# Kernel optimization log

Measured on AMD Instinct MI355X. Metric: run time of the kernel, lower is better.

Reference implementation:

```python
import jax, jax.numpy as jnp
import numpy as np

STD = 0.01

def setup_inputs() -> dict:
    key = jax.random.key(0)
    k1, k2, k3 = jax.random.split(key, 3)
    B, T, D = 16, 4096, 512
    x = jax.random.normal(k1, (B, T, D), dtype=jnp.float32)
    att_W = jax.random.normal(k2, (D, D), dtype=jnp.float32) * STD
    att_v = jax.random.normal(k3, (D,), dtype=jnp.float32) * STD
    return {"x": x, "att_W": att_W, "att_v": att_v}

def reference(x, att_W, att_v):
    # additive attention scores: tanh(x @ W) @ v -> [B, T]
    y = jnp.tanh(jnp.einsum('btd,de->bte', x, att_W))
    scores = jnp.einsum('btd,d->bt', y, att_v)
    weights = jax.nn.softmax(scores, axis=-1)          # softmax over sequence
    out = jnp.einsum('bt,btd->bd', weights, x)         # weighted sum pooling
    return out.astype(jnp.float32)
```

## Files before the change

kernel.cpp:

```cpp
#include <hip/hip_runtime.h>
#include <hip/hip_bf16.h>
#include <math.h>

#define BB 16
#define TT 4096
#define DD 512
#define MM (BB*TT)

typedef __bf16 bf16x8 __attribute__((ext_vector_type(8)));
typedef float  f32x4  __attribute__((ext_vector_type(4)));

__device__ inline unsigned short f2bf(float f) {
    unsigned u = __builtin_bit_cast(unsigned, f) + 0x8000u;
    return (unsigned short)(u >> 16);
}

__device__ inline unsigned pack_bf16x2(float lo, float hi) {
    unsigned u0 = __builtin_bit_cast(unsigned, lo) + 0x8000u;
    unsigned u1 = __builtin_bit_cast(unsigned, hi) + 0x8000u;
    return __builtin_amdgcn_perm(u1, u0, 0x07060302);
}

__device__ inline float tanh_fast(float y) {
    float e = __expf(2.0f * y);
    return 1.0f - 2.0f * __builtin_amdgcn_rcpf(e + 1.0f);
}

__global__ void wb_kernel(const float* __restrict__ W, unsigned short* __restrict__ Wb) {
    int u = blockIdx.x * 256 + threadIdx.x;
    int lane = u & 63;
    int fid  = u >> 6;
    int ni = fid & 1;
    int s  = (fid >> 1) & 15;
    int p  = (fid >> 5) & 7;
    int h  = fid >> 8;
    int n  = h * 256 + p * 32 + ni * 16 + (lane & 15);
    int k0 = s * 32 + (lane >> 4) * 8;
    unsigned short o[8];
    #pragma unroll
    for (int j = 0; j < 8; j++) o[j] = f2bf(W[(size_t)(k0 + j) * DD + n]);
    *(uint4*)(Wb + (size_t)u * 8) = *(uint4*)o;
}

__global__ __launch_bounds__(256, 2) void scorepool_kernel(
        const float* __restrict__ x, const unsigned short* __restrict__ Wb,
        const float* __restrict__ v,
        float* __restrict__ num_ws, float* __restrict__ mz_ws) {
    __shared__ unsigned short As[64 * DD];
    __shared__ float sbuf[4][64];
    __shared__ float ew[64];
    __shared__ float mzsh[2];
    __shared__ float psum[4][DD];

    const int tid  = threadIdx.x;
    const int m0   = blockIdx.x * 64;
    const int wid  = tid >> 6;
    const int lane = tid & 63;
    const int l15  = lane & 15;
    const int q    = lane >> 4;
    const int r3   = l15 & 7;
    const int wh   = wid;

    ((float*)sbuf)[tid] = 0.f;

    #pragma unroll 4
    for (int i = 0; i < 16; i++) {
        int u = i * 256 + tid;
        int r = u >> 6;
        int c = u & 63;
        const float* gp = x + (size_t)(m0 + r) * DD + c * 8;
        f32x4 f0 = __builtin_nontemporal_load((const f32x4*)(gp));
        f32x4 f1 = __builtin_nontemporal_load((const f32x4*)(gp + 4));
        uint4 o;
        o.x = pack_bf16x2(f0.x, f0.y);
        o.y = pack_bf16x2(f0.z, f0.w);
        o.z = pack_bf16x2(f1.x, f1.y);
        o.w = pack_bf16x2(f1.z, f1.w);
        *(uint4*)(&As[r * DD + (c ^ (r & 7)) * 8]) = o;
    }

    const unsigned short* bqp = Wb + (size_t)wh * 65536 + lane * 8;
    bf16x8 b[4][2];
    #pragma unroll
    for (int g = 0; g < 3; g++) {
        b[g][0] = *(const bf16x8*)(bqp);
        b[g][1] = *(const bf16x8*)(bqp + 512);
        bqp += 1024;
    }

    __syncthreads();

#define A_FRAG(mi, s) (*(const bf16x8*)(&As[((mi)*16 + l15) * DD + ((((s)*4 + q) ^ r3) * 8)]))

    bf16x8 a[2][4];
    #pragma unroll
    for (int mi = 0; mi < 4; mi++) a[0][mi] = A_FRAG(mi, 0);

    #pragma unroll 1
    for (int p = 0; p < 4; p++) {
        f32x4 acc[4][2];
        #pragma unroll
        for (int mi = 0; mi < 4; mi++) {
            acc[mi][0] = (f32x4){0.f, 0.f, 0.f, 0.f};
            acc[mi][1] = (f32x4){0.f, 0.f, 0.f, 0.f};
        }

        #pragma unroll
        for (int s = 0; s < 16; s++) {
            const int ns = (s + 1) & 15;
            #pragma unroll
            for (int mi = 0; mi < 4; mi++) a[(s + 1) & 1][mi] = A_FRAG(mi, ns);
            b[(s + 3) & 3][0] = *(const bf16x8*)(bqp);
            b[(s + 3) & 3][1] = *(const bf16x8*)(bqp + 512);
            bqp += 1024;
            #pragma unroll
            for (int mi = 0; mi < 4; mi++)
                #pragma unroll
                for (int ni = 0; ni < 2; ni++)
                    acc[mi][ni] = __builtin_amdgcn_mfma_f32_16x16x32_bf16(
                        a[s & 1][mi], b[s & 3][ni], acc[mi][ni], 0, 0, 0);
        }

        float vv0 = v[wh * 128 + p * 32 + l15];
        float vv1 = v[wh * 128 + p * 32 + 16 + l15];
        #pragma unroll
        for (int mi = 0; mi < 4; mi++)
            #pragma unroll
            for (int rr = 0; rr < 4; rr++) {
                float sum = tanh_fast(acc[mi][0][rr]) * vv0
                          + tanh_fast(acc[mi][1][rr]) * vv1;
                sum += __shfl_xor(sum, 1);
                sum += __shfl_xor(sum, 2);
                sum += __shfl_xor(sum, 4);
                sum += __shfl_xor(sum, 8);
                if (l15 == 0)
                    sbuf[wh][mi * 16 + q * 4 + rr] += sum;
            }
    }
#undef A_FRAG

    __syncthreads();

    if (tid < 64) {
        float s = sbuf[0][tid] + sbuf[1][tid] + sbuf[2][tid] + sbuf[3][tid];
        float m = s;
        #pragma unroll
        for (int off = 32; off; off >>= 1) m = fmaxf(m, __shfl_xor(m, off));
        float e = __expf(s - m);
        float z = e;
        #pragma unroll
        for (int off = 32; off; off >>= 1) z += __shfl_xor(z, off);
        ew[tid] = e;
        if (tid == 0) { mzsh[0] = m; mzsh[1] = z; }
    }
    __syncthreads();

    const int cx = tid & 63;
    const int rg = tid >> 6;
    float nacc[8];
    #pragma unroll
    for (int j = 0; j < 8; j++) nacc[j] = 0.f;
    #pragma unroll 4
    for (int i = 0; i < 16; i++) {
        int r = rg * 16 + i;
        uint4 u = *(const uint4*)(&As[r * DD + ((cx ^ (r & 7)) * 8)]);
        float e = ew[r];
        nacc[0] += e * __builtin_bit_cast(float, u.x << 16);
        nacc[1] += e * __builtin_bit_cast(float, u.x & 0xFFFF0000u);
        nacc[2] += e * __builtin_bit_cast(float, u.y << 16);
        nacc[3] += e * __builtin_bit_cast(float, u.y & 0xFFFF0000u);
        nacc[4] += e * __builtin_bit_cast(float, u.z << 16);
        nacc[5] += e * __builtin_bit_cast(float, u.z & 0xFFFF0000u);
        nacc[6] += e * __builtin_bit_cast(float, u.w << 16);
        nacc[7] += e * __builtin_bit_cast(float, u.w & 0xFFFF0000u);
    }
    *(float4*)(&psum[rg][cx * 8])     = *(float4*)(&nacc[0]);
    *(float4*)(&psum[rg][cx * 8 + 4]) = *(float4*)(&nacc[4]);
    __syncthreads();

    if (tid < 128) {
        int c = tid * 4;
        f32x4 f = *(const f32x4*)(&psum[0][c]);
        f += *(const f32x4*)(&psum[1][c]);
        f += *(const f32x4*)(&psum[2][c]);
        f += *(const f32x4*)(&psum[3][c]);
        __builtin_nontemporal_store(f, (f32x4*)(num_ws + (size_t)blockIdx.x * DD + c));
    }
    if (tid == 0) {
        mz_ws[2 * blockIdx.x]     = mzsh[0];
        mz_ws[2 * blockIdx.x + 1] = mzsh[1];
    }
}

__global__ void combine_kernel(const float* __restrict__ num_ws,
                               const float* __restrict__ mz_ws,
                               float* __restrict__ out) {
    __shared__ float fs[64];
    __shared__ float sinv_sh;
    const int b   = blockIdx.x;
    const int tid = threadIdx.x;

    if (tid < 64) {
        float m = mz_ws[(b * 64 + tid) * 2];
        float z = mz_ws[(b * 64 + tid) * 2 + 1];
        float M = m;
        #pragma unroll
        for (int off = 32; off; off >>= 1) M = fmaxf(M, __shfl_xor(M, off));
        float f  = __expf(m - M);
        float fz = f * z;
        #pragma unroll
        for (int off = 32; off; off >>= 1) fz += __shfl_xor(fz, off);
        fs[tid] = f;
        if (tid == 0) sinv_sh = 1.0f / fz;
    }
    __syncthreads();

    float a0 = 0.f, a1 = 0.f;
    #pragma unroll 4
    for (int c = 0; c < 64; c++) {
        float f = fs[c];
        const float* np = num_ws + (size_t)(b * 64 + c) * DD;
        a0 += f * np[tid];
        a1 += f * np[tid + 256];
    }
    const float sinv = sinv_sh;
    out[b * DD + tid]       = a0 * sinv;
    out[b * DD + tid + 256] = a1 * sinv;
}

extern "C" void kernel_launch(void* const* d_in, const int* in_sizes, int n_in,
                              void* d_out, int out_size, void* d_ws, size_t ws_size,
                              hipStream_t stream) {
    (void)in_sizes; (void)n_in; (void)out_size; (void)ws_size;
    const float* x = (const float*)d_in[0];
    const float* W = (const float*)d_in[1];
    const float* v = (const float*)d_in[2];
    float* out = (float*)d_out;

    unsigned short* Wb = (unsigned short*)d_ws;
    float* num_ws      = (float*)((char*)d_ws + 512 * 1024 + 16 * 1024);
    float* mz_ws       = (float*)((char*)d_ws + 512 * 1024 + 16 * 1024 + 2 * 1024 * 1024);

    wb_kernel<<<128, 256, 0, stream>>>(W, Wb);

    scorepool_kernel<<<MM / 64, 256, 0, stream>>>(x, Wb, v, num_ws, mz_ws);

    combine_kernel<<<BB, 256, 0, stream>>>(num_ws, mz_ws, out);
}
```

Before: 301.6 us.

## Switch score GEMM to 32x32x16 bf16 MFMA with deeper operand prefetch

Replaces the 16x16x32 MFMA tiling, 8 accumulators per wave, with 32x32x16 MFMA using 2 accumulators of 16 floats. W is repacked to the new B-fragment layout and the LDS A-fragment indexing is changed to match. A and B fragments are now prefetched 3 and 7 steps ahead. The aim is fewer MFMA issues and fewer LDS A reads per FLOP, at the cost of an extra shuffle stage in the tanh·v reduction and more registers held for prefetch.

```diff
diff --git a/kernel.cpp b/kernel.cpp
--- a/kernel.cpp
+++ b/kernel.cpp
@@ -9,6 +9,7 @@
 
 typedef __bf16 bf16x8 __attribute__((ext_vector_type(8)));
 typedef float  f32x4  __attribute__((ext_vector_type(4)));
+typedef float  f32x16 __attribute__((ext_vector_type(16)));
 
 __device__ inline unsigned short f2bf(float f) {
     unsigned u = __builtin_bit_cast(unsigned, f) + 0x8000u;
@@ -30,12 +31,11 @@
     int u = blockIdx.x * 256 + threadIdx.x;
     int lane = u & 63;
     int fid  = u >> 6;
-    int ni = fid & 1;
-    int s  = (fid >> 1) & 15;
-    int p  = (fid >> 5) & 7;
-    int h  = fid >> 8;
-    int n  = h * 256 + p * 32 + ni * 16 + (lane & 15);
-    int k0 = s * 32 + (lane >> 4) * 8;
+    int s  = fid & 31;
+    int p  = (fid >> 5) & 3;
+    int qh = fid >> 7;
+    int n  = qh * 128 + p * 32 + (lane & 31);
+    int k0 = s * 16 + (lane >> 5) * 8;
     unsigned short o[8];
     #pragma unroll
     for (int j = 0; j < 8; j++) o[j] = f2bf(W[(size_t)(k0 + j) * DD + n]);
@@ -54,12 +54,11 @@
 
     const int tid  = threadIdx.x;
     const int m0   = blockIdx.x * 64;
-    const int wid  = tid >> 6;
     const int lane = tid & 63;
-    const int l15  = lane & 15;
-    const int q    = lane >> 4;
-    const int r3   = l15 & 7;
-    const int wh   = wid;
+    const int wh   = tid >> 6;
+    const int R    = lane & 31;
+    const int hi   = lane >> 5;
+    const int r7   = R & 7;
 
     ((float*)sbuf)[tid] = 0.f;
 
@@ -80,61 +79,54 @@
     }
 
     const unsigned short* bqp = Wb + (size_t)wh * 65536 + lane * 8;
-    bf16x8 b[4][2];
+    bf16x8 b[8];
+    #pragma unroll
+    for (int g = 0; g < 7; g++) {
+        b[g] = *(const bf16x8*)(bqp);
+        bqp += 512;
+    }
+
+    __syncthreads();
+
+#define A_FRAG(mi, s) (*(const bf16x8*)(&As[((mi) * 32 + R) * DD + ((((s) * 2 + hi) ^ r7) * 8)]))
+
+    bf16x8 a[4][2];
     #pragma unroll
     for (int g = 0; g < 3; g++) {
-        b[g][0] = *(const bf16x8*)(bqp);
-        b[g][1] = *(const bf16x8*)(bqp + 512);
-        bqp += 1024;
-    }
-
-    __syncthreads();
-
-#define A_FRAG(mi, s) (*(const bf16x8*)(&As[((mi)*16 + l15) * DD + ((((s)*4 + q) ^ r3) * 8)]))
-
-    bf16x8 a[2][4];
-    #pragma unroll
-    for (int mi = 0; mi < 4; mi++) a[0][mi] = A_FRAG(mi, 0);
+        a[g][0] = A_FRAG(0, g);
+        a[g][1] = A_FRAG(1, g);
+    }
 
     #pragma unroll 1
     for (int p = 0; p < 4; p++) {
-        f32x4 acc[4][2];
-        #pragma unroll
-        for (int mi = 0; mi < 4; mi++) {
-            acc[mi][0] = (f32x4){0.f, 0.f, 0.f, 0.f};
-            acc[mi][1] = (f32x4){0.f, 0.f, 0.f, 0.f};
+        f32x16 acc[2];
+        #pragma unroll
+        for (int j = 0; j < 16; j++) { acc[0][j] = 0.f; acc[1][j] = 0.f; }
+
+        #pragma unroll
+        for (int s = 0; s < 32; s++) {
+            const int ns = (s + 3) & 31;
+            a[(s + 3) & 3][0] = A_FRAG(0, ns);
+            a[(s + 3) & 3][1] = A_FRAG(1, ns);
+            b[(s + 7) & 7] = *(const bf16x8*)(bqp);
+            bqp += 512;
+            acc[0] = __builtin_amdgcn_mfma_f32_32x32x16_bf16(a[s & 3][0], b[s & 7], acc[0], 0, 0, 0);
+            acc[1] = __builtin_amdgcn_mfma_f32_32x32x16_bf16(a[s & 3][1], b[s & 7], acc[1], 0, 0, 0);
         }
 
-        #pragma unroll
-        for (int s = 0; s < 16; s++) {
-            const int ns = (s + 1) & 15;
+        float vv = v[wh * 128 + p * 32 + R];
+        #pragma unroll
+        for (int mi = 0; mi < 2; mi++)
             #pragma unroll
-            for (int mi = 0; mi < 4; mi++) a[(s + 1) & 1][mi] = A_FRAG(mi, ns);
-            b[(s + 3) & 3][0] = *(const bf16x8*)(bqp);
-            b[(s + 3) & 3][1] = *(const bf16x8*)(bqp + 512);
-            bqp += 1024;
-            #pragma unroll
-            for (int mi = 0; mi < 4; mi++)
-                #pragma unroll
-                for (int ni = 0; ni < 2; ni++)
-                    acc[mi][ni] = __builtin_amdgcn_mfma_f32_16x16x32_bf16(
-                        a[s & 1][mi], b[s & 3][ni], acc[mi][ni], 0, 0, 0);
-        }
-
-        float vv0 = v[wh * 128 + p * 32 + l15];
-        float vv1 = v[wh * 128 + p * 32 + 16 + l15];
-        #pragma unroll
-        for (int mi = 0; mi < 4; mi++)
-            #pragma unroll
-            for (int rr = 0; rr < 4; rr++) {
-                float sum = tanh_fast(acc[mi][0][rr]) * vv0
-                          + tanh_fast(acc[mi][1][rr]) * vv1;
+            for (int reg = 0; reg < 16; reg++) {
+                float sum = tanh_fast(acc[mi][reg]) * vv;
                 sum += __shfl_xor(sum, 1);
                 sum += __shfl_xor(sum, 2);
                 sum += __shfl_xor(sum, 4);
                 sum += __shfl_xor(sum, 8);
-                if (l15 == 0)
-                    sbuf[wh][mi * 16 + q * 4 + rr] += sum;
+                sum += __shfl_xor(sum, 16);
+                if (R == 0)
+                    sbuf[wh][mi * 32 + (reg & 3) + 8 * (reg >> 2) + 4 * hi] += sum;
             }
     }
 #undef A_FRAG
```

Result: slower. 342.7 us (+13.6%).
